# Kernel tuning notes

Measured on AMD Instinct MI355X. Metric: run time of the kernel, lower is better.

The kernel has to match this reference:

```python
import jax, jax.numpy as jnp
import numpy as np

B, INA, H = 128, 128, 32
OUT, SPLIT, K = 512, 4, 3
LEGO = int(OUT * 0.25)  # 128 lego filters
NUM_LABELS = 10


def setup_inputs() -> dict:
    key = jax.random.key(0)
    k1, k2, k3, k4, k5 = jax.random.split(key, 5)
    x = jax.random.normal(k1, (B, INA, H, H), dtype=jnp.float32)
    label = jax.random.randint(k2, (B,), 0, NUM_LABELS)
    # kaiming-normal-ish initializations (fan_in based std)
    ff_std = float(np.sqrt(2.0 / (INA * K * K)))
    first_filter = jax.random.normal(k3, (NUM_LABELS, LEGO, INA, K, K), dtype=jnp.float32) * ff_std
    sc_std = float(np.sqrt(2.0 / LEGO))
    second_filter_coefficients = jax.random.normal(k4, (SPLIT, OUT, LEGO, 1, 1), dtype=jnp.float32) * sc_std
    second_filter_combination = jax.random.normal(k5, (SPLIT, OUT, LEGO, 1, 1), dtype=jnp.float32) * sc_std
    return {
        'x': x,
        'label': label,
        'first_filter': first_filter,
        'second_filter_coefficients': second_filter_coefficients,
        'second_filter_combination': second_filter_combination,
    }


def reference(x, label, first_filter, second_filter_coefficients, second_filter_combination):
    # Gather per-sample first-stage filter bank by label: [B, LEGO, INA, K, K]
    w = first_filter[label]

    # Per-sample conv2d with padding=1 (same spatial size), vectorized via vmap.
    def conv_one(xi, wi):
        # xi: [INA, H, H], wi: [LEGO, INA, K, K]
        return jax.lax.conv_general_dilated(
            xi[None], wi, window_strides=(1, 1), padding=[(1, 1), (1, 1)],
            dimension_numbers=('NCHW', 'OIHW', 'NCHW'))[0]

    feat = jax.vmap(conv_one)(x, w)  # [B, LEGO, H, H]

    # temp_combination: one-hot of argmax over lego dim (STE hard selection); only split index 0 used.
    comb0 = second_filter_combination[0, :, :, 0, 0]            # [OUT, LEGO]
    onehot = jax.nn.one_hot(jnp.argmax(comb0, axis=1), comb0.shape[1], dtype=x.dtype)
    kern = second_filter_coefficients[0, :, :, 0, 0] * onehot   # [OUT, LEGO] masked 1x1 kernel

    # 1x1 conv == channel contraction
    out = jnp.einsum('blhw,ol->bohw', feat, kern)
    return out
```

## Files before the change

kernel.cpp:

```cpp
#include <hip/hip_runtime.h>

typedef float f32x4 __attribute__((ext_vector_type(4)));
typedef short s16x8 __attribute__((ext_vector_type(8)));
typedef short s16x4 __attribute__((ext_vector_type(4)));

#define NLAB 10
#define LEGO 128
#define INA  128
#define OUTC 512
#define KDIM 1152
#define WPITCH 34
#define XL_ELEMS (6*34*128)

__device__ __forceinline__ unsigned short f2bf(float f) {
    unsigned u = __builtin_bit_cast(unsigned, f);
    u += 0x7fffu + ((u >> 16) & 1u);
    return (unsigned short)(u >> 16);
}
__device__ __forceinline__ float bf2f(unsigned short h) {
    return __builtin_bit_cast(float, ((unsigned)h) << 16);
}

__global__ void k_prep_w(const float* __restrict__ ff, unsigned short* __restrict__ wt) {
    int t = blockIdx.x * 256 + threadIdx.x;
    if (t >= NLAB * LEGO * INA) return;
    int ic = t & 127;
    int ll = t >> 7;
    const float* src = ff + (size_t)(ll * 128 + ic) * 9;
    unsigned short* dst = wt + (size_t)ll * KDIM + ic;
#pragma unroll
    for (int off = 0; off < 9; ++off) dst[off * 128] = f2bf(src[off]);
}

__global__ void k_prep_sel(const float* __restrict__ coeff, const float* __restrict__ comb,
                           int* __restrict__ sel, float* __restrict__ cs) {
    int o = blockIdx.x * 256 + threadIdx.x;
    if (o >= OUTC) return;
    const float* row = comb + (size_t)o * LEGO;
    float best = row[0]; int bi = 0;
    for (int l = 1; l < LEGO; ++l) { float v = row[l]; if (v > best) { best = v; bi = l; } }
    sel[o] = bi;
    cs[o] = coeff[(size_t)o * LEGO + bi];
}

__global__ __launch_bounds__(256, 2) void k_conv(
    const float* __restrict__ x, const int* __restrict__ label,
    const unsigned short* __restrict__ wt,
    const int* __restrict__ sel, const float* __restrict__ cs,
    float* __restrict__ out)
{
    __shared__ unsigned short xl[XL_ELEMS];

    const int t  = threadIdx.x;
    const int b  = blockIdx.y;
    const int nt = blockIdx.x;
    const int h0 = nt * 4;

    {
        uint4* z = (uint4*)xl;
        for (int i = t; i < XL_ELEMS/8; i += 256) z[i] = make_uint4(0u,0u,0u,0u);
    }
    __syncthreads();

    const int lab = label[b];

    for (int i = t; i < 6144; i += 256) {
        int wq  = i & 7;
        int ri  = i >> 3;
        int row = ri % 6;
        int ic  = ri / 6;
        int h = h0 - 1 + row;
        if (h >= 0 && h < 32) {
            const f32x4 v = *(const f32x4*)(x + (((size_t)b * INA + ic) << 10) + h * 32 + wq * 4);
            int icl = ic & 7, ich = ic >> 3;
#pragma unroll
            for (int j = 0; j < 4; ++j) {
                int w1 = wq * 4 + j + 1;
                int el = (row * WPITCH + w1) * 128 + (((ich ^ (w1 & 15)) << 3) | icl);
                xl[el] = f2bf(v[j]);
            }
        }
    }
    __syncthreads();

    const int lane = t & 63;
    const int wv   = t >> 6;
    const int l16  = lane & 15;
    const int quad = lane >> 4;
    const int m_base = (wv & 1) << 6;
    const int n_base = (wv >> 1) << 6;

    const unsigned short* wl = wt + (size_t)lab * (LEGO * KDIM);
    const unsigned short* arow[4];
#pragma unroll
    for (int mi = 0; mi < 4; ++mi)
        arow[mi] = wl + (size_t)(m_base + mi*16 + l16) * KDIM + quad * 8;

    int prow[4], pcol[4];
#pragma unroll
    for (int ni = 0; ni < 4; ++ni) {
        int p = n_base + ni*16 + l16;
        prow[ni] = p >> 5;
        pcol[ni] = p & 31;
    }

    f32x4 acc[4][4];
    {
        f32x4 zz = {0.f, 0.f, 0.f, 0.f};
#pragma unroll
        for (int mi = 0; mi < 4; ++mi)
#pragma unroll
            for (int ni = 0; ni < 4; ++ni) acc[mi][ni] = zz;
    }

    s16x8 ap[3][4];
#pragma unroll
    for (int s = 0; s < 2; ++s)
#pragma unroll
        for (int mi = 0; mi < 4; ++mi)
            ap[s][mi] = *(const s16x8*)(arow[mi] + s * 32);

#pragma unroll
    for (int off = 0; off < 9; ++off) {
        const int dh = off / 3 - 1;
        const int dw = off % 3 - 1;
        int bbase[4], bsw[4];
#pragma unroll
        for (int ni = 0; ni < 4; ++ni) {
            int row = prow[ni] + dh + 1;
            int w1  = pcol[ni] + dw + 1;
            bbase[ni] = (row * WPITCH + w1) * 128;
            bsw[ni]   = w1 & 15;
        }
#pragma unroll
        for (int kc = 0; kc < 4; ++kc) {
            const int step = off * 4 + kc;
            if (step + 2 < 36) {
#pragma unroll
                for (int mi = 0; mi < 4; ++mi)
                    ap[(step + 2) % 3][mi] = *(const s16x8*)(arow[mi] + (step + 2) * 32);
            }
            const int jj = kc * 4 + quad;
            s16x8 bb[4];
#pragma unroll
            for (int ni = 0; ni < 4; ++ni)
                bb[ni] = *(const s16x8*)(xl + bbase[ni] + ((jj ^ bsw[ni]) << 3));
            const s16x8* a = ap[step % 3];
#pragma unroll
            for (int mi = 0; mi < 4; ++mi)
#pragma unroll
                for (int ni = 0; ni < 4; ++ni)
                    acc[mi][ni] = __builtin_amdgcn_mfma_f32_16x16x32_bf16(a[mi], bb[ni], acc[mi][ni], 0, 0, 0);
        }
    }

    __syncthreads();
    unsigned short* featb = xl;
#pragma unroll
    for (int mi = 0; mi < 4; ++mi)
#pragma unroll
        for (int ni = 0; ni < 4; ++ni) {
            int n = n_base + ni*16 + l16;
#pragma unroll
            for (int r = 0; r < 4; ++r) {
                int m = m_base + mi*16 + quad*4 + r;
                featb[m * 132 + n] = f2bf(acc[mi][ni][r]);
            }
        }
    __syncthreads();

    const size_t obase = ((size_t)b * OUTC) * 1024 + (size_t)nt * 128;
    for (int i = t; i < OUTC * 32; i += 256) {
        int pg = i & 31;
        int o  = i >> 5;
        int so = sel[o];
        float cc = cs[o];
        s16x4 fv = *(const s16x4*)(featb + so * 132 + pg * 4);
        f32x4 ov;
#pragma unroll
        for (int j = 0; j < 4; ++j)
            ov[j] = cc * bf2f((unsigned short)fv[j]);
        __builtin_nontemporal_store(ov, (f32x4*)(out + obase + (size_t)o * 1024 + pg * 4));
    }
}

extern "C" void kernel_launch(void* const* d_in, const int* in_sizes, int n_in,
                              void* d_out, int out_size, void* d_ws, size_t ws_size,
                              hipStream_t stream) {
    const float* x     = (const float*)d_in[0];
    const int*   label = (const int*)d_in[1];
    const float* ff    = (const float*)d_in[2];
    const float* coeff = (const float*)d_in[3];
    const float* comb  = (const float*)d_in[4];
    float* out = (float*)d_out;

    char* ws = (char*)d_ws;
    unsigned short* wt = (unsigned short*)ws;
    int*   sel = (int*)(ws + 2949120);
    float* cs  = (float*)(ws + 2949120 + 2048);

    k_prep_w  <<<640, 256, 0, stream>>>(ff, wt);
    k_prep_sel<<<2,   256, 0, stream>>>(coeff, comb, sel, cs);
    k_conv    <<<dim3(8, 128), 256, 0, stream>>>(x, label, wt, sel, cs, out);
}
```

Baseline: 412.5 us.

## Pre-convert input to padded swizzled bf16 and DMA tiles into LDS

Adds a prep kernel that converts x to a zero-padded, swizzled bf16 layout in workspace. The conv kernel then loads its 6-row halo tile with global_load_lds direct-to-LDS transfers instead of per-element float loads, conversion and scattered LDS stores. The weight register prefetch now overlaps with the tile load, and occupancy is raised to 3 blocks per CU. The cost is an extra kernel launch and an extra ~38MB bf16 write and read of the input. The old path is kept as a fallback when the workspace is too small.

```diff
diff --git a/kernel.cpp b/kernel.cpp
--- a/kernel.cpp
+++ b/kernel.cpp
@@ -10,7 +10,8 @@
 #define OUTC 512
 #define KDIM 1152
 #define WPITCH 34
-#define XL_ELEMS (6*34*128)
+#define XROW (WPITCH * 128)
+#define XL_ELEMS (6 * XROW)
 
 __device__ __forceinline__ unsigned short f2bf(float f) {
     unsigned u = __builtin_bit_cast(unsigned, f);
@@ -19,6 +20,12 @@
 }
 __device__ __forceinline__ float bf2f(unsigned short h) {
     return __builtin_bit_cast(float, ((unsigned)h) << 16);
+}
+
+__device__ __forceinline__ void g2l16(const void* g, void* l) {
+    __builtin_amdgcn_global_load_lds(
+        (const __attribute__((address_space(1))) void*)g,
+        (__attribute__((address_space(3))) void*)l, 16, 0, 0);
 }
 
 __global__ void k_prep_w(const float* __restrict__ ff, unsigned short* __restrict__ wt) {
@@ -43,7 +50,164 @@
     cs[o] = coeff[(size_t)o * LEGO + bi];
 }
 
-__global__ __launch_bounds__(256, 2) void k_conv(
+__global__ __launch_bounds__(256, 4) void k_prep_x(
+    const float* __restrict__ x, unsigned short* __restrict__ xbf)
+{
+    const int r = blockIdx.x, b = blockIdx.y, t = threadIdx.x;
+    unsigned short* dst = xbf + ((size_t)b * 34 + r) * XROW;
+    if (r == 0 || r == 33) {
+        uint4* z = (uint4*)dst;
+        for (int i = t; i < XROW / 8; i += 256) z[i] = make_uint4(0u,0u,0u,0u);
+        return;
+    }
+    __shared__ float sx[128][33];
+    const int h = r - 1;
+    for (int c = t; c < 1024; c += 256) {
+        int ic = c >> 3, wq = c & 7;
+        f32x4 v = *(const f32x4*)(x + (((size_t)b * INA + ic) << 10) + h * 32 + wq * 4);
+#pragma unroll
+        for (int j = 0; j < 4; ++j) sx[ic][wq * 4 + j] = v[j];
+    }
+    __syncthreads();
+    for (int task = t; task < 512; task += 256) {
+        int w1 = (task >> 4) + 1;
+        int g  = task & 15;
+        int sg = g ^ (w1 & 15);
+        int w  = w1 - 1;
+        s16x8 o;
+#pragma unroll
+        for (int k = 0; k < 8; ++k) o[k] = (short)f2bf(sx[sg * 8 + k][w]);
+        *(s16x8*)(dst + (w1 << 7) + (g << 3)) = o;
+    }
+    if (t < 32) {
+        int w1 = (t & 1) ? 33 : 0;
+        int g  = t >> 1;
+        s16x8 zz = {0,0,0,0,0,0,0,0};
+        *(s16x8*)(dst + (w1 << 7) + (g << 3)) = zz;
+    }
+}
+
+__global__ __launch_bounds__(256, 3) void k_conv_dma(
+    const unsigned short* __restrict__ xbf, const int* __restrict__ label,
+    const unsigned short* __restrict__ wt,
+    const int* __restrict__ sel, const float* __restrict__ cs,
+    float* __restrict__ out)
+{
+    __shared__ unsigned short xl[XL_ELEMS];
+
+    const int t  = threadIdx.x;
+    const int b  = blockIdx.y;
+    const int nt = blockIdx.x;
+    const int lane = t & 63;
+    const int wv   = t >> 6;
+
+    const unsigned short* src = xbf + ((size_t)b * 34 + nt * 4) * XROW;
+    for (int c = wv; c < 51; c += 4)
+        g2l16(src + (c << 9) + (lane << 3), xl + (c << 9));
+
+    const int lab = label[b];
+    const int l16  = lane & 15;
+    const int quad = lane >> 4;
+    const int m_base = (wv & 1) << 6;
+    const int n_base = (wv >> 1) << 6;
+
+    const unsigned short* wl = wt + (size_t)lab * (LEGO * KDIM);
+    const unsigned short* arow[4];
+#pragma unroll
+    for (int mi = 0; mi < 4; ++mi)
+        arow[mi] = wl + (size_t)(m_base + mi*16 + l16) * KDIM + quad * 8;
+
+    int prow[4], pcol[4];
+#pragma unroll
+    for (int ni = 0; ni < 4; ++ni) {
+        int p = n_base + ni*16 + l16;
+        prow[ni] = p >> 5;
+        pcol[ni] = p & 31;
+    }
+
+    f32x4 acc[4][4];
+    {
+        f32x4 zz = {0.f, 0.f, 0.f, 0.f};
+#pragma unroll
+        for (int mi = 0; mi < 4; ++mi)
+#pragma unroll
+            for (int ni = 0; ni < 4; ++ni) acc[mi][ni] = zz;
+    }
+
+    s16x8 ap[3][4];
+#pragma unroll
+    for (int s = 0; s < 2; ++s)
+#pragma unroll
+        for (int mi = 0; mi < 4; ++mi)
+            ap[s][mi] = *(const s16x8*)(arow[mi] + s * 32);
+
+    __syncthreads();
+
+#pragma unroll
+    for (int off = 0; off < 9; ++off) {
+        const int dh = off / 3 - 1;
+        const int dw = off % 3 - 1;
+        int bbase[4], bsw[4];
+#pragma unroll
+        for (int ni = 0; ni < 4; ++ni) {
+            int row = prow[ni] + dh + 1;
+            int w1  = pcol[ni] + dw + 1;
+            bbase[ni] = (row * WPITCH + w1) * 128;
+            bsw[ni]   = w1 & 15;
+        }
+#pragma unroll
+        for (int kc = 0; kc < 4; ++kc) {
+            const int step = off * 4 + kc;
+            if (step + 2 < 36) {
+#pragma unroll
+                for (int mi = 0; mi < 4; ++mi)
+                    ap[(step + 2) % 3][mi] = *(const s16x8*)(arow[mi] + (step + 2) * 32);
+            }
+            const int jj = kc * 4 + quad;
+            s16x8 bb[4];
+#pragma unroll
+            for (int ni = 0; ni < 4; ++ni)
+                bb[ni] = *(const s16x8*)(xl + bbase[ni] + ((jj ^ bsw[ni]) << 3));
+            const s16x8* a = ap[step % 3];
+#pragma unroll
+            for (int mi = 0; mi < 4; ++mi)
+#pragma unroll
+                for (int ni = 0; ni < 4; ++ni)
+                    acc[mi][ni] = __builtin_amdgcn_mfma_f32_16x16x32_bf16(a[mi], bb[ni], acc[mi][ni], 0, 0, 0);
+        }
+    }
+
+    __syncthreads();
+    unsigned short* featb = xl;
+#pragma unroll
+    for (int mi = 0; mi < 4; ++mi)
+#pragma unroll
+        for (int ni = 0; ni < 4; ++ni) {
+            int n = n_base + ni*16 + l16;
+#pragma unroll
+            for (int r = 0; r < 4; ++r) {
+                int m = m_base + mi*16 + quad*4 + r;
+                featb[m * 132 + n] = f2bf(acc[mi][ni][r]);
+            }
+        }
+    __syncthreads();
+
+    const size_t obase = ((size_t)b * OUTC) * 1024 + (size_t)nt * 128;
+    for (int i = t; i < OUTC * 32; i += 256) {
+        int pg = i & 31;
+        int o  = i >> 5;
+        int so = sel[o];
+        float cc = cs[o];
+        s16x4 fv = *(const s16x4*)(featb + so * 132 + pg * 4);
+        f32x4 ov;
+#pragma unroll
+        for (int j = 0; j < 4; ++j)
+            ov[j] = cc * bf2f((unsigned short)fv[j]);
+        __builtin_nontemporal_store(ov, (f32x4*)(out + obase + (size_t)o * 1024 + pg * 4));
+    }
+}
+
+__global__ __launch_bounds__(256, 2) void k_conv_old(
     const float* __restrict__ x, const int* __restrict__ label,
     const unsigned short* __restrict__ wt,
     const int* __restrict__ sel, const float* __restrict__ cs,
@@ -195,11 +359,20 @@
     float* out = (float*)d_out;
 
     char* ws = (char*)d_ws;
-    unsigned short* wt = (unsigned short*)ws;
+    unsigned short* wt  = (unsigned short*)ws;
     int*   sel = (int*)(ws + 2949120);
     float* cs  = (float*)(ws + 2949120 + 2048);
+    unsigned short* xbf = (unsigned short*)(ws + 2949120 + 4096);
+
+    const size_t need = 2949120ull + 4096ull + 37879808ull;
 
     k_prep_w  <<<640, 256, 0, stream>>>(ff, wt);
     k_prep_sel<<<2,   256, 0, stream>>>(coeff, comb, sel, cs);
-    k_conv    <<<dim3(8, 128), 256, 0, stream>>>(x, label, wt, sel, cs, out);
-}
+
+    if (ws_size >= need) {
+        k_prep_x <<<dim3(34, 128), 256, 0, stream>>>(x, xbf);
+        k_conv_dma<<<dim3(8, 128), 256, 0, stream>>>(xbf, label, wt, sel, cs, out);
+    } else {
+        k_conv_old<<<dim3(8, 128), 256, 0, stream>>>(x, label, wt, sel, cs, out);
+    }
+}
```

After: 415.3 us. Within noise of the previous version (+0.7%).

## Halve conv spatial tile, double grid, merge prep kernels, cache sel in LDS

Applied to the files above, without the earlier changes.

The conv tile shrinks from 4 output rows to 2 (64 pixels). Each wave now covers 32 lego channels across all 64 pixels, and the grid doubles to 16x128 blocks with launch bounds raised to 4 blocks per CU. This cuts LDS and register use per block so more blocks fit per CU. The two prep kernels are merged into one launch, and sel/cs are staged into shared memory for the epilogue. In exchange, the halo share of the x loads grows and each B fragment is reused by fewer A rows, so arithmetic intensity drops.

```diff
diff --git a/kernel.cpp b/kernel.cpp
--- a/kernel.cpp
+++ b/kernel.cpp
@@ -10,7 +10,8 @@
 #define OUTC 512
 #define KDIM 1152
 #define WPITCH 34
-#define XL_ELEMS (6*34*128)
+#define XROWS 4
+#define XL_ELEMS (XROWS * WPITCH * 128)
 
 __device__ __forceinline__ unsigned short f2bf(float f) {
     unsigned u = __builtin_bit_cast(unsigned, f);
@@ -21,20 +22,23 @@
     return __builtin_bit_cast(float, ((unsigned)h) << 16);
 }
 
-__global__ void k_prep_w(const float* __restrict__ ff, unsigned short* __restrict__ wt) {
-    int t = blockIdx.x * 256 + threadIdx.x;
-    if (t >= NLAB * LEGO * INA) return;
-    int ic = t & 127;
-    int ll = t >> 7;
-    const float* src = ff + (size_t)(ll * 128 + ic) * 9;
-    unsigned short* dst = wt + (size_t)ll * KDIM + ic;
-#pragma unroll
-    for (int off = 0; off < 9; ++off) dst[off * 128] = f2bf(src[off]);
-}
-
-__global__ void k_prep_sel(const float* __restrict__ coeff, const float* __restrict__ comb,
-                           int* __restrict__ sel, float* __restrict__ cs) {
-    int o = blockIdx.x * 256 + threadIdx.x;
+__global__ void k_prep(const float* __restrict__ ff,
+                       const float* __restrict__ coeff, const float* __restrict__ comb,
+                       unsigned short* __restrict__ wt,
+                       int* __restrict__ sel, float* __restrict__ cs) {
+    const int gb = blockIdx.x;
+    if (gb < 640) {
+        int t = gb * 256 + threadIdx.x;
+        if (t >= NLAB * LEGO * INA) return;
+        int ic = t & 127;
+        int ll = t >> 7;
+        const float* src = ff + (size_t)(ll * 128 + ic) * 9;
+        unsigned short* dst = wt + (size_t)ll * KDIM + ic;
+#pragma unroll
+        for (int off = 0; off < 9; ++off) dst[off * 128] = f2bf(src[off]);
+        return;
+    }
+    int o = (gb - 640) * 256 + threadIdx.x;
     if (o >= OUTC) return;
     const float* row = comb + (size_t)o * LEGO;
     float best = row[0]; int bi = 0;
@@ -43,32 +47,36 @@
     cs[o] = coeff[(size_t)o * LEGO + bi];
 }
 
-__global__ __launch_bounds__(256, 2) void k_conv(
+__global__ __launch_bounds__(256, 4) void k_conv2(
     const float* __restrict__ x, const int* __restrict__ label,
     const unsigned short* __restrict__ wt,
     const int* __restrict__ sel, const float* __restrict__ cs,
     float* __restrict__ out)
 {
     __shared__ unsigned short xl[XL_ELEMS];
+    __shared__ int   s_sel[OUTC];
+    __shared__ float s_cs[OUTC];
 
     const int t  = threadIdx.x;
     const int b  = blockIdx.y;
     const int nt = blockIdx.x;
-    const int h0 = nt * 4;
+    const int h0 = nt * 2;
+
+    for (int i = t; i < OUTC; i += 256) { s_sel[i] = sel[i]; s_cs[i] = cs[i]; }
 
     {
         uint4* z = (uint4*)xl;
-        for (int i = t; i < XL_ELEMS/8; i += 256) z[i] = make_uint4(0u,0u,0u,0u);
+        for (int i = t; i < XL_ELEMS / 8; i += 256) z[i] = make_uint4(0u,0u,0u,0u);
     }
     __syncthreads();
 
     const int lab = label[b];
 
-    for (int i = t; i < 6144; i += 256) {
+    for (int i = t; i < 4096; i += 256) {
         int wq  = i & 7;
         int ri  = i >> 3;
-        int row = ri % 6;
-        int ic  = ri / 6;
+        int row = ri & 3;
+        int ic  = ri >> 2;
         int h = h0 - 1 + row;
         if (h >= 0 && h < 32) {
             const f32x4 v = *(const f32x4*)(x + (((size_t)b * INA + ic) << 10) + h * 32 + wq * 4);
@@ -87,37 +95,36 @@
     const int wv   = t >> 6;
     const int l16  = lane & 15;
     const int quad = lane >> 4;
-    const int m_base = (wv & 1) << 6;
-    const int n_base = (wv >> 1) << 6;
+    const int m_base = wv << 5;
 
     const unsigned short* wl = wt + (size_t)lab * (LEGO * KDIM);
-    const unsigned short* arow[4];
-#pragma unroll
-    for (int mi = 0; mi < 4; ++mi)
+    const unsigned short* arow[2];
+#pragma unroll
+    for (int mi = 0; mi < 2; ++mi)
         arow[mi] = wl + (size_t)(m_base + mi*16 + l16) * KDIM + quad * 8;
 
     int prow[4], pcol[4];
 #pragma unroll
     for (int ni = 0; ni < 4; ++ni) {
-        int p = n_base + ni*16 + l16;
+        int p = ni*16 + l16;
         prow[ni] = p >> 5;
         pcol[ni] = p & 31;
     }
 
-    f32x4 acc[4][4];
+    f32x4 acc[2][4];
     {
         f32x4 zz = {0.f, 0.f, 0.f, 0.f};
 #pragma unroll
-        for (int mi = 0; mi < 4; ++mi)
+        for (int mi = 0; mi < 2; ++mi)
 #pragma unroll
             for (int ni = 0; ni < 4; ++ni) acc[mi][ni] = zz;
     }
 
-    s16x8 ap[3][4];
-#pragma unroll
-    for (int s = 0; s < 2; ++s)
-#pragma unroll
-        for (int mi = 0; mi < 4; ++mi)
+    s16x8 ap[4][2];
+#pragma unroll
+    for (int s = 0; s < 3; ++s)
+#pragma unroll
+        for (int mi = 0; mi < 2; ++mi)
             ap[s][mi] = *(const s16x8*)(arow[mi] + s * 32);
 
 #pragma unroll
@@ -135,19 +142,19 @@
 #pragma unroll
         for (int kc = 0; kc < 4; ++kc) {
             const int step = off * 4 + kc;
-            if (step + 2 < 36) {
-#pragma unroll
-                for (int mi = 0; mi < 4; ++mi)
-                    ap[(step + 2) % 3][mi] = *(const s16x8*)(arow[mi] + (step + 2) * 32);
+            if (step + 3 < 36) {
+#pragma unroll
+                for (int mi = 0; mi < 2; ++mi)
+                    ap[(step + 3) & 3][mi] = *(const s16x8*)(arow[mi] + (step + 3) * 32);
             }
             const int jj = kc * 4 + quad;
             s16x8 bb[4];
 #pragma unroll
             for (int ni = 0; ni < 4; ++ni)
                 bb[ni] = *(const s16x8*)(xl + bbase[ni] + ((jj ^ bsw[ni]) << 3));
-            const s16x8* a = ap[step % 3];
-#pragma unroll
-            for (int mi = 0; mi < 4; ++mi)
+            const s16x8* a = ap[step & 3];
+#pragma unroll
+            for (int mi = 0; mi < 2; ++mi)
 #pragma unroll
                 for (int ni = 0; ni < 4; ++ni)
                     acc[mi][ni] = __builtin_amdgcn_mfma_f32_16x16x32_bf16(a[mi], bb[ni], acc[mi][ni], 0, 0, 0);
@@ -157,25 +164,25 @@
     __syncthreads();
     unsigned short* featb = xl;
 #pragma unroll
-    for (int mi = 0; mi < 4; ++mi)
+    for (int mi = 0; mi < 2; ++mi)
 #pragma unroll
         for (int ni = 0; ni < 4; ++ni) {
-            int n = n_base + ni*16 + l16;
+            int n = ni*16 + l16;
 #pragma unroll
             for (int r = 0; r < 4; ++r) {
                 int m = m_base + mi*16 + quad*4 + r;
-                featb[m * 132 + n] = f2bf(acc[mi][ni][r]);
+                featb[m * 68 + n] = f2bf(acc[mi][ni][r]);
             }
         }
     __syncthreads();
 
-    const size_t obase = ((size_t)b * OUTC) * 1024 + (size_t)nt * 128;
-    for (int i = t; i < OUTC * 32; i += 256) {
-        int pg = i & 31;
-        int o  = i >> 5;
-        int so = sel[o];
-        float cc = cs[o];
-        s16x4 fv = *(const s16x4*)(featb + so * 132 + pg * 4);
+    const size_t obase = ((size_t)b * OUTC) * 1024 + (size_t)h0 * 32;
+    for (int i = t; i < OUTC * 16; i += 256) {
+        int pg = i & 15;
+        int o  = i >> 4;
+        int so = s_sel[o];
+        float cc = s_cs[o];
+        s16x4 fv = *(const s16x4*)(featb + so * 68 + pg * 4);
         f32x4 ov;
 #pragma unroll
         for (int j = 0; j < 4; ++j)
@@ -195,11 +202,10 @@
     float* out = (float*)d_out;
 
     char* ws = (char*)d_ws;
-    unsigned short* wt = (unsigned short*)ws;
+    unsigned short* wt  = (unsigned short*)ws;
     int*   sel = (int*)(ws + 2949120);
     float* cs  = (float*)(ws + 2949120 + 2048);
 
-    k_prep_w  <<<640, 256, 0, stream>>>(ff, wt);
-    k_prep_sel<<<2,   256, 0, stream>>>(coeff, comb, sel, cs);
-    k_conv    <<<dim3(8, 128), 256, 0, stream>>>(x, label, wt, sel, cs, out);
-}
+    k_prep <<<642, 256, 0, stream>>>(ff, coeff, comb, wt, sel, cs);
+    k_conv2<<<dim3(16, 128), 256, 0, stream>>>(x, label, wt, sel, cs, out);
+}
```

Measured after the change: 441.3 us. 7.0% more time.

## Vectorize input staging, zero only halo, merge prep kernels, raise occupancy

Applied to the files above, without the earlier changes.

The two prep kernels are merged into a single launch with block-index dispatch. In the conv kernel, only the halo columns and the boundary rows of the LDS tile are zeroed, not the whole tile, and one barrier is removed. Each thread now loads 8 input channels and writes packed 16-byte bf16 vectors to LDS instead of scalar shorts. Launch bounds rise to 3 blocks per CU. Together these cut staging instructions, LDS write traffic and launch overhead, at the risk of register pressure under the tighter occupancy bound.

```diff
diff --git a/kernel.cpp b/kernel.cpp
--- a/kernel.cpp
+++ b/kernel.cpp
@@ -21,20 +21,23 @@
     return __builtin_bit_cast(float, ((unsigned)h) << 16);
 }
 
-__global__ void k_prep_w(const float* __restrict__ ff, unsigned short* __restrict__ wt) {
-    int t = blockIdx.x * 256 + threadIdx.x;
-    if (t >= NLAB * LEGO * INA) return;
-    int ic = t & 127;
-    int ll = t >> 7;
-    const float* src = ff + (size_t)(ll * 128 + ic) * 9;
-    unsigned short* dst = wt + (size_t)ll * KDIM + ic;
-#pragma unroll
-    for (int off = 0; off < 9; ++off) dst[off * 128] = f2bf(src[off]);
-}
-
-__global__ void k_prep_sel(const float* __restrict__ coeff, const float* __restrict__ comb,
-                           int* __restrict__ sel, float* __restrict__ cs) {
-    int o = blockIdx.x * 256 + threadIdx.x;
+__global__ void k_prep(const float* __restrict__ ff,
+                       const float* __restrict__ coeff, const float* __restrict__ comb,
+                       unsigned short* __restrict__ wt,
+                       int* __restrict__ sel, float* __restrict__ cs) {
+    const int gb = blockIdx.x;
+    if (gb < 640) {
+        int t = gb * 256 + threadIdx.x;
+        if (t >= NLAB * LEGO * INA) return;
+        int ic = t & 127;
+        int ll = t >> 7;
+        const float* src = ff + (size_t)(ll * 128 + ic) * 9;
+        unsigned short* dst = wt + (size_t)ll * KDIM + ic;
+#pragma unroll
+        for (int off = 0; off < 9; ++off) dst[off * 128] = f2bf(src[off]);
+        return;
+    }
+    int o = (gb - 640) * 256 + threadIdx.x;
     if (o >= OUTC) return;
     const float* row = comb + (size_t)o * LEGO;
     float best = row[0]; int bi = 0;
@@ -43,7 +46,7 @@
     cs[o] = coeff[(size_t)o * LEGO + bi];
 }
 
-__global__ __launch_bounds__(256, 2) void k_conv(
+__global__ __launch_bounds__(256, 3) void k_conv(
     const float* __restrict__ x, const int* __restrict__ label,
     const unsigned short* __restrict__ wt,
     const int* __restrict__ sel, const float* __restrict__ cs,
@@ -57,31 +60,46 @@
     const int h0 = nt * 4;
 
     {
-        uint4* z = (uint4*)xl;
-        for (int i = t; i < XL_ELEMS/8; i += 256) z[i] = make_uint4(0u,0u,0u,0u);
-    }
-    __syncthreads();
+        s16x8 zz = {0,0,0,0,0,0,0,0};
+        if (t < 192) {
+            int row = t >> 5;
+            int c   = (t >> 1) & 15;
+            int w1  = (t & 1) ? 33 : 0;
+            *(s16x8*)(xl + (row * WPITCH + w1) * 128 + c * 8) = zz;
+        }
+        if (nt == 0)
+            for (int i = t; i < 544; i += 256)
+                *(s16x8*)(xl + (0 * WPITCH + (i >> 4)) * 128 + (i & 15) * 8) = zz;
+        if (nt == 7)
+            for (int i = t; i < 544; i += 256)
+                *(s16x8*)(xl + (5 * WPITCH + (i >> 4)) * 128 + (i & 15) * 8) = zz;
+    }
 
     const int lab = label[b];
 
-    for (int i = t; i < 6144; i += 256) {
-        int wq  = i & 7;
-        int ri  = i >> 3;
-        int row = ri % 6;
-        int ic  = ri / 6;
+    for (int it = 0; it < 3; ++it) {
+        int idx = t + it * 256;
+        int wq  = idx & 7;
+        int gg  = (idx >> 3) & 15;
+        int row = idx >> 7;
         int h = h0 - 1 + row;
         if (h >= 0 && h < 32) {
-            const f32x4 v = *(const f32x4*)(x + (((size_t)b * INA + ic) << 10) + h * 32 + wq * 4);
-            int icl = ic & 7, ich = ic >> 3;
+            f32x4 vv[8];
+            const float* xb = x + ((size_t)b * INA) * 1024 + h * 32 + wq * 4;
+#pragma unroll
+            for (int k = 0; k < 8; ++k)
+                vv[k] = *(const f32x4*)(xb + (size_t)(gg * 8 + k) * 1024);
 #pragma unroll
             for (int j = 0; j < 4; ++j) {
                 int w1 = wq * 4 + j + 1;
-                int el = (row * WPITCH + w1) * 128 + (((ich ^ (w1 & 15)) << 3) | icl);
-                xl[el] = f2bf(v[j]);
+                int c  = gg ^ (w1 & 15);
+                s16x8 o;
+#pragma unroll
+                for (int k = 0; k < 8; ++k) o[k] = (short)f2bf(vv[k][j]);
+                *(s16x8*)(xl + (row * WPITCH + w1) * 128 + c * 8) = o;
             }
         }
     }
-    __syncthreads();
 
     const int lane = t & 63;
     const int wv   = t >> 6;
@@ -119,6 +137,8 @@
 #pragma unroll
         for (int mi = 0; mi < 4; ++mi)
             ap[s][mi] = *(const s16x8*)(arow[mi] + s * 32);
+
+    __syncthreads();
 
 #pragma unroll
     for (int off = 0; off < 9; ++off) {
@@ -195,11 +215,10 @@
     float* out = (float*)d_out;
 
     char* ws = (char*)d_ws;
-    unsigned short* wt = (unsigned short*)ws;
+    unsigned short* wt  = (unsigned short*)ws;
     int*   sel = (int*)(ws + 2949120);
     float* cs  = (float*)(ws + 2949120 + 2048);
 
-    k_prep_w  <<<640, 256, 0, stream>>>(ff, wt);
-    k_prep_sel<<<2,   256, 0, stream>>>(coeff, comb, sel, cs);
-    k_conv    <<<dim3(8, 128), 256, 0, stream>>>(x, label, wt, sel, cs, out);
-}
+    k_prep<<<642, 256, 0, stream>>>(ff, coeff, comb, wt, sel, cs);
+    k_conv<<<dim3(8, 128), 256, 0, stream>>>(x, label, wt, sel, cs, out);
+}
```

Result: no change. 406.5 us (-1.5%).
